# Kernel tuning notes

Measured on AMD Instinct MI355X. Metric: run time of the kernel, lower is better.

## Reference

```python
import jax, jax.numpy as jnp
import numpy as np

ALPHA = 0.2  # leaky_relu slope from GATLayer
NEG_INF = -9e15


def gat_layer(h, W, a, adj_mask, concat):
    """Faithful GATLayer.forward without the NxNx2F intermediate.

    h: [b, N, Fin], W: [Fin, Fout], a: [2*Fout], adj_mask: [b, N, N] bool.
    e[b,i,j] = leaky_relu(a[:F].Wh_i + a[F:].Wh_j)  (same math as torch concat version).
    """
    Wh = jnp.einsum('bnf,fo->bno', h, W)            # [b, N, Fout]
    Fo = W.shape[1]
    e1 = Wh @ a[:Fo]                                 # [b, N]  (source term)
    e2 = Wh @ a[Fo:]                                 # [b, N]  (target term)
    e = e1[:, :, None] + e2[:, None, :]              # [b, N, N]
    e = jax.nn.leaky_relu(e, negative_slope=ALPHA)
    e = jnp.where(adj_mask, e, NEG_INF)
    attn = jax.nn.softmax(e, axis=2)                 # softmax over neighbors j
    out = jnp.einsum('bij,bjo->bio', attn, Wh)       # [b, N, Fout]
    return jax.nn.elu(out) if concat else out


def setup_inputs() -> dict:
    key = jax.random.key(0)
    ks = jax.random.split(key, 6)
    b, N = 32, 512
    comp_dim, gat_dim, num_head = 80, 50, 3
    h = jax.random.normal(ks[0], (b, N, comp_dim), dtype=jnp.float32)
    adj = jax.random.randint(ks[1], (b, N, N), 0, 2, dtype=jnp.int32)
    s = 1.414 / np.sqrt(comp_dim)
    Ws = jax.random.uniform(ks[2], (num_head, comp_dim, gat_dim), jnp.float32, -s, s)
    attn_a = jax.random.uniform(ks[3], (num_head, 2 * gat_dim), jnp.float32, -0.2, 0.2)
    so = 1.414 / np.sqrt(gat_dim * num_head)
    W_out = jax.random.uniform(ks[4], (gat_dim * num_head, comp_dim), jnp.float32, -so, so)
    a_out = jax.random.uniform(ks[5], (2 * comp_dim,), jnp.float32, -0.15, 0.15)
    return {"h": h, "adj": adj, "Ws": Ws, "attn_a": attn_a, "W_out": W_out, "a_out": a_out}


def reference(h, adj, Ws, attn_a, W_out, a_out):
    adj_mask = adj > 0
    # num_head parallel GAT heads (concat=True), vmapped over the head axis
    heads = jax.vmap(lambda W, a: gat_layer(h, W, a, adj_mask, True))(Ws, attn_a)
    # [H, b, N, gat_dim] -> [b, N, H*gat_dim]
    Hn, b, N, Fo = heads.shape
    cat = jnp.transpose(heads, (1, 2, 0, 3)).reshape(b, N, Hn * Fo)
    # output GAT layer (concat=False -> no ELU)
    return gat_layer(cat, W_out, a_out, adj_mask, False)
```

## Files before the change

### kernel.cpp

```cpp
#include <hip/hip_runtime.h>
#include <stdint.h>

typedef unsigned long long u64;
typedef __attribute__((ext_vector_type(8))) short short8;
typedef __attribute__((ext_vector_type(4))) float f32x4;

#define B_ 32
#define N_ 512
#define FIN_ 80
#define FH_ 50
#define FO_ 80
#define CAT_ 150
#define KP_ 160
#define NP_ 96

__device__ inline unsigned short f2bf(float f) {
  unsigned u = __float_as_uint(f);
  u += 0x7fffu + ((u >> 16) & 1u);
  return (unsigned short)(u >> 16);
}

__device__ inline unsigned nib4(int4 v) {
  return (v.x != 0 ? 1u : 0u) | (v.y != 0 ? 2u : 0u) |
         (v.z != 0 ? 4u : 0u) | (v.w != 0 ? 8u : 0u);
}

__device__ inline short8 build_af(const float* e2s, float e1r, u64 word,
                                  int jb, int shift) {
  short8 af;
  unsigned b0 = (unsigned)(word >> shift) & 0xffu;
  float4 va = *(const float4*)&e2s[jb];
  float4 vb = *(const float4*)&e2s[jb + 4];
  float ev[8] = {va.x, va.y, va.z, va.w, vb.x, vb.y, vb.z, vb.w};
  #pragma unroll
  for (int e = 0; e < 8; ++e) {
    float sv = e1r + ev[e];
    sv = fmaxf(sv, 0.2f * sv);
    sv = fminf(sv, 60.f);
    float arg = ((b0 >> e) & 1u) ? sv : -1e30f;
    af[e] = (short)f2bf(__expf(arg));
  }
  return af;
}

__global__ __launch_bounds__(256) void k0_maskprep(const int* __restrict__ adj,
                                                   const float* __restrict__ Wout,
                                                   const float* __restrict__ a_out,
                                                   u64* __restrict__ maskw,
                                                   unsigned short* __restrict__ WoutT,
                                                   float* __restrict__ wv1,
                                                   float* __restrict__ wv2) {
  __shared__ unsigned short sm[256];
  const int t = threadIdx.x;
  const int bid = blockIdx.x;

  if (bid < 2048) {
    const int r = t >> 5, s = t & 31;
    const int row = bid * 8 + r;
    const int4* src = (const int4*)(adj + (size_t)row * N_ + s * 16);
    int4 v0 = src[0], v1 = src[1], v2 = src[2], v3 = src[3];
    unsigned m = nib4(v0) | (nib4(v1) << 4) | (nib4(v2) << 8) | (nib4(v3) << 12);
    sm[t] = (unsigned short)m;
    __syncthreads();
    if (t < 64) {
      const int rr = t >> 3, w = t & 7;
      const unsigned short* p = &sm[rr * 32 + w * 4];
      u64 mm = (u64)p[0] | ((u64)p[1] << 16) | ((u64)p[2] << 32) | ((u64)p[3] << 48);
      maskw[(size_t)(bid * 8 + rr) * 8 + w] = mm;
    }
    return;
  }
  if (bid < 2063) {
    const int i = (bid - 2048) * 256 + t;
    const int base = i * 4;
    const int col = base / KP_, k0 = base % KP_;
    unsigned short pk[4];
    #pragma unroll
    for (int e = 0; e < 4; ++e) {
      const int k = k0 + e;
      pk[e] = (col < FO_ && k < CAT_) ? f2bf(Wout[(size_t)k * FO_ + col]) : 0;
    }
    uint2 o;
    o.x = (unsigned)pk[0] | ((unsigned)pk[1] << 16);
    o.y = (unsigned)pk[2] | ((unsigned)pk[3] << 16);
    ((uint2*)WoutT)[i] = o;
    return;
  }
  if (t < CAT_) {
    const float4* wr = (const float4*)(Wout + (size_t)t * FO_);
    const float4* a1 = (const float4*)a_out;
    const float4* a2 = (const float4*)(a_out + FO_);
    float p1 = 0.f, p2 = 0.f;
    #pragma unroll
    for (int i = 0; i < 20; ++i) {
      float4 v = wr[i], x1 = a1[i], x2 = a2[i];
      p1 += v.x * x1.x + v.y * x1.y + v.z * x1.z + v.w * x1.w;
      p2 += v.x * x2.x + v.y * x2.y + v.z * x2.z + v.w * x2.w;
    }
    wv1[t] = p1; wv2[t] = p2;
  }
}

__global__ __launch_bounds__(256) void k1_mfma(const float* __restrict__ h,
                                               const float* __restrict__ Ws,
                                               const float* __restrict__ attn_a,
                                               unsigned short* __restrict__ whT,
                                               float* __restrict__ e1h,
                                               float* __restrict__ e2h) {
  __shared__ __align__(16) unsigned short un[64 * 104];
  __shared__ __align__(16) unsigned short bstage[12 * 512];
  const int t = threadIdx.x;
  int x = blockIdx.x;
  const int rt = x & 7; x >>= 3;
  const int bb = x & 31; x >>= 5;
  const int hh = x;
  const int n0 = rt * 64;
  const float* hblk = h + ((size_t)bb * N_ + n0) * FIN_;
  const float* wsrc = Ws + (size_t)hh * FIN_ * FH_;

  for (int idx = t; idx < 64 * 13; idx += 256) {
    const int row = idx / 13, k0 = (idx - row * 13) * 8;
    short8 v8;
    if (k0 < FIN_) {
      float4 a = *(const float4*)(hblk + row * FIN_ + k0);
      float4 b = *(const float4*)(hblk + row * FIN_ + k0 + 4);
      v8[0] = (short)f2bf(a.x); v8[1] = (short)f2bf(a.y);
      v8[2] = (short)f2bf(a.z); v8[3] = (short)f2bf(a.w);
      v8[4] = (short)f2bf(b.x); v8[5] = (short)f2bf(b.y);
      v8[6] = (short)f2bf(b.z); v8[7] = (short)f2bf(b.w);
    } else {
      #pragma unroll
      for (int e = 0; e < 8; ++e) v8[e] = 0;
    }
    *(short8*)&un[row * 104 + k0] = v8;
  }
  for (int idx = t; idx < 768; idx += 256) {
    const int f = idx >> 6, lf = idx & 63;
    const int ks = f >> 2, nt = f & 3;
    const int kb = ks * 32 + (lf >> 4) * 8, n = nt * 16 + (lf & 15);
    short8 v8;
    #pragma unroll
    for (int e = 0; e < 8; ++e) {
      const int k = kb + e;
      v8[e] = (k < FIN_ && n < FH_) ? (short)f2bf(wsrc[k * FH_ + n]) : (short)0;
    }
    *(short8*)&bstage[idx * 8] = v8;
  }
  __syncthreads();

  const int l = t & 63, wv = t >> 6, q = l >> 4, rl = l & 15;
  f32x4 acc[4];
  {
    short8 af[3];
    #pragma unroll
    for (int ks = 0; ks < 3; ++ks)
      af[ks] = *(const short8*)&un[(wv * 16 + rl) * 104 + ks * 32 + q * 8];
    #pragma unroll
    for (int nt = 0; nt < 4; ++nt) acc[nt] = (f32x4){0.f, 0.f, 0.f, 0.f};
    #pragma unroll
    for (int ks = 0; ks < 3; ++ks)
      #pragma unroll
      for (int nt = 0; nt < 4; ++nt)
        acc[nt] = __builtin_amdgcn_mfma_f32_16x16x32_bf16(
            af[ks], *(const short8*)&bstage[((ks * 4 + nt) * 64 + l) * 8], acc[nt], 0, 0, 0);
  }
  {
    float a1v[4], a2v[4];
    #pragma unroll
    for (int c = 0; c < 4; ++c) {
      const int col = c * 16 + rl;
      a1v[c] = (col < FH_) ? attn_a[hh * 2 * FH_ + col] : 0.f;
      a2v[c] = (col < FH_) ? attn_a[hh * 2 * FH_ + FH_ + col] : 0.f;
    }
    #pragma unroll
    for (int r = 0; r < 4; ++r) {
      float p1 = acc[0][r] * a1v[0] + acc[1][r] * a1v[1] +
                 acc[2][r] * a1v[2] + acc[3][r] * a1v[3];
      float p2 = acc[0][r] * a2v[0] + acc[1][r] * a2v[1] +
                 acc[2][r] * a2v[2] + acc[3][r] * a2v[3];
      p1 += __shfl_xor(p1, 1); p1 += __shfl_xor(p1, 2);
      p1 += __shfl_xor(p1, 4); p1 += __shfl_xor(p1, 8);
      p2 += __shfl_xor(p2, 1); p2 += __shfl_xor(p2, 2);
      p2 += __shfl_xor(p2, 4); p2 += __shfl_xor(p2, 8);
      if (rl == 0) {
        size_t o = ((size_t)hh * B_ + bb) * N_ + n0 + wv * 16 + q * 4 + r;
        e1h[o] = p1; e2h[o] = p2;
      }
    }
  }
  __syncthreads();
  unsigned short* tbT = un;
  #pragma unroll
  for (int nt = 0; nt < 4; ++nt)
    #pragma unroll
    for (int r2 = 0; r2 < 4; ++r2)
      tbT[(nt * 16 + rl) * 72 + wv * 16 + q * 4 + r2] = f2bf(acc[nt][r2]);
  __syncthreads();
  {
    const int col = t & 63, half = t >> 6;
    uint4 o0 = *(const uint4*)&tbT[col * 72 + half * 16];
    uint4 o1 = *(const uint4*)&tbT[col * 72 + half * 16 + 8];
    if (col == 63) {
      o0.x = o0.y = o0.z = o0.w = 0x3f803f80u;
      o1 = o0;
    }
    unsigned short* dst = whT + (((size_t)hh * B_ + bb) * 64 + col) * 512 + n0 + half * 16;
    *(uint4*)dst = o0;
    *(uint4*)(dst + 8) = o1;
  }
}

__global__ __launch_bounds__(256) void k3s(const unsigned short* __restrict__ whT,
                                           const float* __restrict__ e1,
                                           const float* __restrict__ e2,
                                           const u64* __restrict__ maskw,
                                           const float* __restrict__ wv1,
                                           const float* __restrict__ wv2,
                                           unsigned short* __restrict__ catT,
                                           float* __restrict__ e1p,
                                           float* __restrict__ e2p) {
  __shared__ __align__(16) float e2s[N_];
  __shared__ __align__(16) float red[4][64][17];
  int x = (int)((blockIdx.x & 7) * 384 + (blockIdx.x >> 3));
  const int hh = x >> 10;
  const int bb = (x >> 5) & 31;
  const int rg = x & 31;
  const int n0 = rg * 16;
  const int t = threadIdx.x;
  const int l = t & 63, wid = t >> 6;
  const int q = l >> 4, rl = l & 15;

  const float* e2pp = e2 + ((size_t)hh * B_ + bb) * N_;
  for (int i = t; i < N_ / 4; i += 256) ((float4*)e2s)[i] = ((const float4*)e2pp)[i];
  __syncthreads();

  const int row = n0 + rl;
  const float e1r = e1[((size_t)hh * B_ + bb) * N_ + row];
  const u64* mr = maskw + ((size_t)bb * N_ + row) * 8;

  f32x4 acc[4];
  #pragma unroll
  for (int c = 0; c < 4; ++c) acc[c] = (f32x4){0.f, 0.f, 0.f, 0.f};
  const unsigned short* wb = whT + ((size_t)hh * B_ + bb) * 64 * 512;

  #pragma unroll
  for (int tts = 0; tts < 2; ++tts) {
    const int tt = wid * 2 + tts;
    short8 bf[4][2];
    #pragma unroll
    for (int c = 0; c < 4; ++c) {
      const unsigned short* bp = wb + (size_t)(c * 16 + rl) * 512 + tt * 64 + q * 8;
      bf[c][0] = *(const short8*)bp;
      bf[c][1] = *(const short8*)(bp + 32);
    }
    u64 word = mr[tt];
    short8 af0 = build_af(e2s, e1r, word, tt * 64 + q * 8, q * 8);
    short8 af1 = build_af(e2s, e1r, word, tt * 64 + 32 + q * 8, 32 + q * 8);
    #pragma unroll
    for (int c = 0; c < 4; ++c) {
      acc[c] = __builtin_amdgcn_mfma_f32_16x16x32_bf16(af0, bf[c][0], acc[c], 0, 0, 0);
      acc[c] = __builtin_amdgcn_mfma_f32_16x16x32_bf16(af1, bf[c][1], acc[c], 0, 0, 0);
    }
  }

  #pragma unroll
  for (int c = 0; c < 4; ++c)
    #pragma unroll
    for (int r = 0; r < 4; ++r) red[wid][l][c * 4 + r] = acc[c][r];
  __syncthreads();

  if (wid == 0) {
    #pragma unroll
    for (int c = 0; c < 4; ++c)
      #pragma unroll
      for (int r = 0; r < 4; ++r)
        acc[c][r] = red[0][l][c * 4 + r] + red[1][l][c * 4 + r] +
                    red[2][l][c * 4 + r] + red[3][l][c * 4 + r];
    float w1c[4], w2c[4];
    #pragma unroll
    for (int c = 0; c < 4; ++c) {
      const int col = c * 16 + rl;
      w1c[c] = (col < FH_) ? wv1[hh * FH_ + col] : 0.f;
      w2c[c] = (col < FH_) ? wv2[hh * FH_ + col] : 0.f;
    }
    #pragma unroll
    for (int r = 0; r < 4; ++r) {
      float srow = __shfl(acc[3][r], (q << 4) | 15);
      float invr = srow > 0.f ? 1.f / srow : 0.f;
      const int jrow = n0 + q * 4 + r;
      const size_t grow = (size_t)bb * N_ + jrow;
      float p1 = 0.f, p2 = 0.f;
      #pragma unroll
      for (int c = 0; c < 4; ++c) {
        const int col = c * 16 + rl;
        if (col < FH_) {
          float v = acc[c][r] * invr;
          v = v > 0.f ? v : __expf(v) - 1.f;
          catT[((size_t)bb * KP_ + hh * FH_ + col) * 512 + jrow] = f2bf(v);
          p1 += v * w1c[c];
          p2 += v * w2c[c];
        }
      }
      p1 += __shfl_xor(p1, 1); p1 += __shfl_xor(p1, 2);
      p1 += __shfl_xor(p1, 4); p1 += __shfl_xor(p1, 8);
      p2 += __shfl_xor(p2, 1); p2 += __shfl_xor(p2, 2);
      p2 += __shfl_xor(p2, 4); p2 += __shfl_xor(p2, 8);
      if (rl == 0) {
        e1p[(size_t)hh * (B_ * N_) + grow] = p1;
        e2p[(size_t)hh * (B_ * N_) + grow] = p2;
      }
    }
  }
  if (hh == 2 && t < 16) {
    const int j = n0 + t;
    #pragma unroll
    for (int kc = CAT_; kc < KP_; ++kc)
      catT[((size_t)bb * KP_ + kc) * 512 + j] = (kc == KP_ - 1) ? (unsigned short)0x3f80 : 0;
  }
}

__global__ __launch_bounds__(256) void kC(const unsigned short* __restrict__ catT,
                                          const unsigned short* __restrict__ WoutT,
                                          const float* __restrict__ e1p,
                                          const float* __restrict__ e2p,
                                          const u64* __restrict__ maskw,
                                          float* __restrict__ out) {
  __shared__ __align__(16) float e2s[N_];
  __shared__ __align__(16) float red[3][64][41];
  __shared__ __align__(16) unsigned short pA[16 * 168];
  __shared__ float denomLDS[16];
  int x = (int)((blockIdx.x & 7) * 128 + (blockIdx.x >> 3));
  const int rg = x & 31;
  const int bb = x >> 5;
  const int n0 = rg * 16;
  const int t = threadIdx.x;
  const int l = t & 63, wid = t >> 6;
  const int q = l >> 4, rl = l & 15;

  for (int i = t; i < N_ / 4; i += 256) {
    float4 v0 = ((const float4*)(e2p))[(size_t)bb * 128 + i];
    float4 v1 = ((const float4*)(e2p + B_ * N_))[(size_t)bb * 128 + i];
    float4 v2 = ((const float4*)(e2p + 2 * B_ * N_))[(size_t)bb * 128 + i];
    float4 s;
    s.x = v0.x + v1.x + v2.x; s.y = v0.y + v1.y + v2.y;
    s.z = v0.z + v1.z + v2.z; s.w = v0.w + v1.w + v2.w;
    ((float4*)e2s)[i] = s;
  }
  __syncthreads();

  const int row = n0 + rl;
  const size_t gr = (size_t)bb * N_ + row;
  const float e1r = e1p[gr] + e1p[B_ * N_ + gr] + e1p[2 * B_ * N_ + gr];
  const u64* mr = maskw + gr * 8;

  f32x4 acc[10];
  #pragma unroll
  for (int c = 0; c < 10; ++c) acc[c] = (f32x4){0.f, 0.f, 0.f, 0.f};
  const unsigned short* cb = catT + (size_t)bb * KP_ * 512;

  #pragma unroll
  for (int tts = 0; tts < 2; ++tts) {
    const int tt = wid * 2 + tts;
    u64 word = mr[tt];
    short8 af0 = build_af(e2s, e1r, word, tt * 64 + q * 8, q * 8);
    short8 af1 = build_af(e2s, e1r, word, tt * 64 + 32 + q * 8, 32 + q * 8);
    #pragma unroll
    for (int c = 0; c < 10; ++c) {
      const unsigned short* bp = cb + (size_t)(c * 16 + rl) * 512 + tt * 64 + q * 8;
      short8 b0 = *(const short8*)bp;
      short8 b1 = *(const short8*)(bp + 32);
      acc[c] = __builtin_amdgcn_mfma_f32_16x16x32_bf16(af0, b0, acc[c], 0, 0, 0);
      acc[c] = __builtin_amdgcn_mfma_f32_16x16x32_bf16(af1, b1, acc[c], 0, 0, 0);
    }
  }

  if (wid > 0) {
    #pragma unroll
    for (int c = 0; c < 10; ++c)
      #pragma unroll
      for (int r = 0; r < 4; ++r) red[wid - 1][l][c * 4 + r] = acc[c][r];
  }
  __syncthreads();

  if (wid == 0) {
    #pragma unroll
    for (int c = 0; c < 10; ++c)
      #pragma unroll
      for (int r = 0; r < 4; ++r) {
        const int idx = c * 4 + r;
        acc[c][r] += red[0][l][idx] + red[1][l][idx] + red[2][l][idx];
      }
    #pragma unroll
    for (int c = 0; c < 10; ++c)
      #pragma unroll
      for (int r = 0; r < 4; ++r)
        pA[(q * 4 + r) * 168 + c * 16 + rl] = f2bf(acc[c][r]);
    if (rl == 15) {
      #pragma unroll
      for (int r = 0; r < 4; ++r) denomLDS[q * 4 + r] = acc[9][r];
    }
  }
  __syncthreads();

  if (wid == 0) {
    short8 af2[5];
    #pragma unroll
    for (int ks = 0; ks < 5; ++ks)
      af2[ks] = *(const short8*)&pA[rl * 168 + ks * 32 + q * 8];
    f32x4 acc2[5];
    #pragma unroll
    for (int nt = 0; nt < 5; ++nt) acc2[nt] = (f32x4){0.f, 0.f, 0.f, 0.f};
    #pragma unroll
    for (int ks = 0; ks < 5; ++ks)
      #pragma unroll
      for (int nt = 0; nt < 5; ++nt)
        acc2[nt] = __builtin_amdgcn_mfma_f32_16x16x32_bf16(
            af2[ks],
            *(const short8*)&WoutT[(size_t)(nt * 16 + rl) * KP_ + ks * 32 + q * 8],
            acc2[nt], 0, 0, 0);
    #pragma unroll
    for (int r = 0; r < 4; ++r) {
      const float dv = denomLDS[q * 4 + r];
      const float invr = dv > 0.f ? 1.f / dv : 0.f;
      const size_t ob = ((size_t)bb * N_ + n0 + q * 4 + r) * FO_;
      #pragma unroll
      for (int nt = 0; nt < 5; ++nt) out[ob + nt * 16 + rl] = acc2[nt][r] * invr;
    }
  }
}

extern "C" void kernel_launch(void* const* d_in, const int* in_sizes, int n_in,
                              void* d_out, int out_size, void* d_ws, size_t ws_size,
                              hipStream_t stream) {
  const float* h    = (const float*)d_in[0];
  const int*   adj  = (const int*)d_in[1];
  const float* Ws   = (const float*)d_in[2];
  const float* aa   = (const float*)d_in[3];
  const float* Wout = (const float*)d_in[4];
  const float* aout = (const float*)d_in[5];

  char* ws = (char*)d_ws;
  unsigned short* whT   = (unsigned short*)(ws + 0);
  float* e1h            = (float*)(ws + 6291456);
  float* e2h            = (float*)(ws + 6488064);
  u64*   mk             = (u64*)  (ws + 6684672);
  unsigned short* catT  = (unsigned short*)(ws + 7733248);
  unsigned short* WoutT = (unsigned short*)(ws + 12976128);
  float* wv1            = (float*)(ws + 13008896);
  float* wv2            = (float*)(ws + 13009920);
  float* e1p            = (float*)(ws + 13010944);
  float* e2p            = (float*)(ws + 13207552);

  hipLaunchKernelGGL(k0_maskprep, dim3(2064), dim3(256), 0, stream,
                     adj, Wout, aout, mk, WoutT, wv1, wv2);
  hipLaunchKernelGGL(k1_mfma, dim3(768), dim3(256), 0, stream,
                     h, Ws, aa, whT, e1h, e2h);
  hipLaunchKernelGGL(k3s, dim3(3072), dim3(256), 0, stream,
                     whT, e1h, e2h, mk, wv1, wv2, catT, e1p, e2p);
  hipLaunchKernelGGL(kC, dim3(1024), dim3(256), 0, stream,
                     catT, WoutT, e1p, e2p, mk, (float*)d_out);
}
```

Baseline: 78.32 us.

## Give each k3s wave its own rows and spread kC output GEMM across waves

k3s now assigns each of its four waves a separate 16-row tile and walks the full 512-neighbour K range per wave. This replaces the old split-K across waves and drops the LDS reduction buffer, the extra barrier and the single-wave epilogue; the grid shrinks from 3072 to 768 blocks. In kC the final Wout MFMA stage is distributed across the waves by output tile instead of running on wave 0 only. The padding writes now set only the last catT row to one and no longer zero rows 150-158, which relies on those rows already being zero.

```diff
diff --git a/kernel.cpp b/kernel.cpp
--- a/kernel.cpp
+++ b/kernel.cpp
@@ -220,12 +220,11 @@
                                            float* __restrict__ e1p,
                                            float* __restrict__ e2p) {
   __shared__ __align__(16) float e2s[N_];
-  __shared__ __align__(16) float red[4][64][17];
-  int x = (int)((blockIdx.x & 7) * 384 + (blockIdx.x >> 3));
-  const int hh = x >> 10;
-  const int bb = (x >> 5) & 31;
-  const int rg = x & 31;
-  const int n0 = rg * 16;
+  int x = (int)((blockIdx.x & 7) * 96 + (blockIdx.x >> 3));
+  const int rt = x & 7; x >>= 3;
+  const int bb = x & 31; x >>= 5;
+  const int hh = x;
+  const int n0 = rt * 64;
   const int t = threadIdx.x;
   const int l = t & 63, wid = t >> 6;
   const int q = l >> 4, rl = l & 15;
@@ -234,7 +233,7 @@
   for (int i = t; i < N_ / 4; i += 256) ((float4*)e2s)[i] = ((const float4*)e2pp)[i];
   __syncthreads();
 
-  const int row = n0 + rl;
+  const int row = n0 + wid * 16 + rl;
   const float e1r = e1[((size_t)hh * B_ + bb) * N_ + row];
   const u64* mr = maskw + ((size_t)bb * N_ + row) * 8;
 
@@ -243,9 +242,7 @@
   for (int c = 0; c < 4; ++c) acc[c] = (f32x4){0.f, 0.f, 0.f, 0.f};
   const unsigned short* wb = whT + ((size_t)hh * B_ + bb) * 64 * 512;
 
-  #pragma unroll
-  for (int tts = 0; tts < 2; ++tts) {
-    const int tt = wid * 2 + tts;
+  for (int tt = 0; tt < 8; ++tt) {
     short8 bf[4][2];
     #pragma unroll
     for (int c = 0; c < 4; ++c) {
@@ -263,60 +260,42 @@
     }
   }
 
-  #pragma unroll
-  for (int c = 0; c < 4; ++c)
-    #pragma unroll
-    for (int r = 0; r < 4; ++r) red[wid][l][c * 4 + r] = acc[c][r];
-  __syncthreads();
-
-  if (wid == 0) {
-    #pragma unroll
-    for (int c = 0; c < 4; ++c)
-      #pragma unroll
-      for (int r = 0; r < 4; ++r)
-        acc[c][r] = red[0][l][c * 4 + r] + red[1][l][c * 4 + r] +
-                    red[2][l][c * 4 + r] + red[3][l][c * 4 + r];
-    float w1c[4], w2c[4];
+  float w1c[4], w2c[4];
+  #pragma unroll
+  for (int c = 0; c < 4; ++c) {
+    const int col = c * 16 + rl;
+    w1c[c] = (col < FH_) ? wv1[hh * FH_ + col] : 0.f;
+    w2c[c] = (col < FH_) ? wv2[hh * FH_ + col] : 0.f;
+  }
+  #pragma unroll
+  for (int r = 0; r < 4; ++r) {
+    float srow = __shfl(acc[3][r], (q << 4) | 15);
+    float invr = srow > 0.f ? 1.f / srow : 0.f;
+    const int jrow = n0 + wid * 16 + q * 4 + r;
+    const size_t grow = (size_t)bb * N_ + jrow;
+    float p1 = 0.f, p2 = 0.f;
     #pragma unroll
     for (int c = 0; c < 4; ++c) {
       const int col = c * 16 + rl;
-      w1c[c] = (col < FH_) ? wv1[hh * FH_ + col] : 0.f;
-      w2c[c] = (col < FH_) ? wv2[hh * FH_ + col] : 0.f;
-    }
-    #pragma unroll
-    for (int r = 0; r < 4; ++r) {
-      float srow = __shfl(acc[3][r], (q << 4) | 15);
-      float invr = srow > 0.f ? 1.f / srow : 0.f;
-      const int jrow = n0 + q * 4 + r;
-      const size_t grow = (size_t)bb * N_ + jrow;
-      float p1 = 0.f, p2 = 0.f;
-      #pragma unroll
-      for (int c = 0; c < 4; ++c) {
-        const int col = c * 16 + rl;
-        if (col < FH_) {
-          float v = acc[c][r] * invr;
-          v = v > 0.f ? v : __expf(v) - 1.f;
-          catT[((size_t)bb * KP_ + hh * FH_ + col) * 512 + jrow] = f2bf(v);
-          p1 += v * w1c[c];
-          p2 += v * w2c[c];
-        }
+      if (col < FH_) {
+        float v = acc[c][r] * invr;
+        v = v > 0.f ? v : __expf(v) - 1.f;
+        catT[((size_t)bb * KP_ + hh * FH_ + col) * 512 + jrow] = f2bf(v);
+        p1 += v * w1c[c];
+        p2 += v * w2c[c];
       }
-      p1 += __shfl_xor(p1, 1); p1 += __shfl_xor(p1, 2);
-      p1 += __shfl_xor(p1, 4); p1 += __shfl_xor(p1, 8);
-      p2 += __shfl_xor(p2, 1); p2 += __shfl_xor(p2, 2);
-      p2 += __shfl_xor(p2, 4); p2 += __shfl_xor(p2, 8);
-      if (rl == 0) {
-        e1p[(size_t)hh * (B_ * N_) + grow] = p1;
-        e2p[(size_t)hh * (B_ * N_) + grow] = p2;
-      }
-    }
-  }
-  if (hh == 2 && t < 16) {
-    const int j = n0 + t;
-    #pragma unroll
-    for (int kc = CAT_; kc < KP_; ++kc)
-      catT[((size_t)bb * KP_ + kc) * 512 + j] = (kc == KP_ - 1) ? (unsigned short)0x3f80 : 0;
-  }
+    }
+    p1 += __shfl_xor(p1, 1); p1 += __shfl_xor(p1, 2);
+    p1 += __shfl_xor(p1, 4); p1 += __shfl_xor(p1, 8);
+    p2 += __shfl_xor(p2, 1); p2 += __shfl_xor(p2, 2);
+    p2 += __shfl_xor(p2, 4); p2 += __shfl_xor(p2, 8);
+    if (rl == 0) {
+      e1p[(size_t)hh * (B_ * N_) + grow] = p1;
+      e2p[(size_t)hh * (B_ * N_) + grow] = p2;
+    }
+  }
+  if (hh == 2 && t < 64)
+    catT[((size_t)bb * KP_ + (KP_ - 1)) * 512 + n0 + t] = (unsigned short)0x3f80;
 }
 
 __global__ __launch_bounds__(256) void kC(const unsigned short* __restrict__ catT,
@@ -402,29 +381,24 @@
   }
   __syncthreads();
 
-  if (wid == 0) {
+  for (int nt = wid; nt < 5; nt += 4) {
     short8 af2[5];
     #pragma unroll
     for (int ks = 0; ks < 5; ++ks)
       af2[ks] = *(const short8*)&pA[rl * 168 + ks * 32 + q * 8];
-    f32x4 acc2[5];
-    #pragma unroll
-    for (int nt = 0; nt < 5; ++nt) acc2[nt] = (f32x4){0.f, 0.f, 0.f, 0.f};
+    f32x4 acc2 = (f32x4){0.f, 0.f, 0.f, 0.f};
     #pragma unroll
     for (int ks = 0; ks < 5; ++ks)
-      #pragma unroll
-      for (int nt = 0; nt < 5; ++nt)
-        acc2[nt] = __builtin_amdgcn_mfma_f32_16x16x32_bf16(
-            af2[ks],
-            *(const short8*)&WoutT[(size_t)(nt * 16 + rl) * KP_ + ks * 32 + q * 8],
-            acc2[nt], 0, 0, 0);
+      acc2 = __builtin_amdgcn_mfma_f32_16x16x32_bf16(
+          af2[ks],
+          *(const short8*)&WoutT[(size_t)(nt * 16 + rl) * KP_ + ks * 32 + q * 8],
+          acc2, 0, 0, 0);
     #pragma unroll
     for (int r = 0; r < 4; ++r) {
       const float dv = denomLDS[q * 4 + r];
       const float invr = dv > 0.f ? 1.f / dv : 0.f;
       const size_t ob = ((size_t)bb * N_ + n0 + q * 4 + r) * FO_;
-      #pragma unroll
-      for (int nt = 0; nt < 5; ++nt) out[ob + nt * 16 + rl] = acc2[nt][r] * invr;
+      out[ob + nt * 16 + rl] = acc2[r] * invr;
     }
   }
 }
@@ -455,7 +429,7 @@
                      adj, Wout, aout, mk, WoutT, wv1, wv2);
   hipLaunchKernelGGL(k1_mfma, dim3(768), dim3(256), 0, stream,
                      h, Ws, aa, whT, e1h, e2h);
-  hipLaunchKernelGGL(k3s, dim3(3072), dim3(256), 0, stream,
+  hipLaunchKernelGGL(k3s, dim3(768), dim3(256), 0, stream,
                      whT, e1h, e2h, mk, wv1, wv2, catT, e1p, e2p);
   hipLaunchKernelGGL(kC, dim3(1024), dim3(256), 0, stream,
                      catT, WoutT, e1p, e2p, mk, (float*)d_out);
```

New measurement: 78.46 us. Within noise of the previous version (+0.2%).
